# Kernel tuning notes

Measured on AMD Instinct MI355X. Metric: run time of the kernel, lower is better.

The kernel has to match this reference:

```python
import jax, jax.numpy as jnp
import numpy as np

C = 128         # sphere_channels
H = 512         # hidden_channels
EC = 128        # edge_channels
LMAX = 4
K = 4           # num_experts
N_EQ = 2        # ceil(K/2) equivariant experts
N_NE = 2
N_NODES = 8192
N_EDGES = 262144
DEG_SIZES = np.array([2 * l + 1 for l in range(LMAX + 1)])  # [1,3,5,7,9]
M = int(DEG_SIZES.sum())  # 25 coeffs


def setup_inputs() -> dict:
    key = jax.random.key(0)
    ks = jax.random.split(key, 20)
    s = 0.02
    return {
        "x_emb": jax.random.normal(ks[0], (N_NODES, M, C), jnp.float32),
        "t_ij": jax.random.normal(ks[1], (N_EDGES, EC), jnp.float32),
        "edge_index": jax.random.randint(ks[2], (2, N_EDGES), 0, N_NODES, jnp.int32),
        # equivariant experts (stacked on leading expert axis)
        "eq_w1": jax.random.normal(ks[3], (N_EQ, C, H), jnp.float32) * s,
        "eq_gate_w": jax.random.normal(ks[4], (N_EQ, EC, H * (LMAX + 1)), jnp.float32) * s,
        "eq_gate_b": jax.random.normal(ks[5], (N_EQ, H * (LMAX + 1)), jnp.float32) * s,
        "eq_w2": jax.random.normal(ks[6], (N_EQ, H, C), jnp.float32) * s,
        # non-equivariant experts
        "ne_w1": jax.random.normal(ks[7], (N_NE, C, H), jnp.float32) * s,
        "ne_b1": jax.random.normal(ks[8], (N_NE, H), jnp.float32) * s,
        "ne_gate_w": jax.random.normal(ks[9], (N_NE, EC, H), jnp.float32) * s,
        "ne_gate_b": jax.random.normal(ks[10], (N_NE, H), jnp.float32) * s,
        "ne_w2": jax.random.normal(ks[11], (N_NE, H, C), jnp.float32) * s,
        "ne_b2": jax.random.normal(ks[12], (N_NE, C), jnp.float32) * s,
        # router
        "r_w1": jax.random.normal(ks[13], (EC, EC), jnp.float32) * s,
        "r_b1": jax.random.normal(ks[14], (EC,), jnp.float32) * s,
        "r_w2": jax.random.normal(ks[15], (EC, K), jnp.float32) * s,
        "r_b2": jax.random.normal(ks[16], (K,), jnp.float32) * s,
    }


def reference(x_emb, t_ij, edge_index, eq_w1, eq_gate_w, eq_gate_b, eq_w2,
              ne_w1, ne_b1, ne_gate_w, ne_gate_b, ne_w2, ne_b2,
              r_w1, r_b1, r_w2, r_b2):
    N = x_emb.shape[0]
    silu = jax.nn.silu

    # c_i = scatter-mean of t_ij onto destination nodes
    dst = edge_index[1]
    sums = jax.ops.segment_sum(t_ij, dst, num_segments=N)
    cnt = jax.ops.segment_sum(jnp.ones((t_ij.shape[0],), t_ij.dtype), dst, num_segments=N)
    c = sums / jnp.maximum(cnt, 1.0)[:, None]  # [N, EC]

    # soft routing weights from context
    w = jax.nn.softmax(silu(c @ r_w1 + r_b1) @ r_w2 + r_b2, axis=-1)  # [N, K]

    repeats = jnp.asarray(DEG_SIZES)
    is_scalar = (jnp.arange(M) == 0)[:, None]  # l=0 coeff mask, [M,1]

    # --- equivariant experts (vectorized over expert axis e) ---
    h = jnp.einsum('nmc,ech->enmh', x_emb, eq_w1)                      # [e,N,M,H]
    g = silu(jnp.einsum('nc,ecg->eng', c, eq_gate_w) + eq_gate_b[:, None, :])
    g = g.reshape(N_EQ, N, LMAX + 1, H)
    g = jnp.repeat(g, repeats, axis=2, total_repeat_length=M)          # [e,N,M,H]
    h = jnp.where(is_scalar, silu(h), h) * g                           # SiLU only on l=0
    out_eq = jnp.einsum('enmh,ehc->enmc', h, eq_w2)

    # --- non-equivariant experts ---
    h2 = silu(jnp.einsum('nmc,ech->enmh', x_emb, ne_w1) + ne_b1[:, None, None, :])
    g2 = silu(jnp.einsum('nc,ech->enh', c, ne_gate_w) + ne_gate_b[:, None, :])
    h2 = h2 * g2[:, :, None, :]
    out_ne = jnp.einsum('enmh,ehc->enmc', h2, ne_w2) + ne_b2[:, None, None, :]

    # softmax-weighted mixture (equiv experts first, matching ModuleList order)
    out = (jnp.einsum('nk,knmc->nmc', w[:, :N_EQ], out_eq)
           + jnp.einsum('nk,knmc->nmc', w[:, N_EQ:], out_ne))
    return out
```

## Files before the change

kernel.cpp:

```cpp
#include <hip/hip_runtime.h>

#define NNODES 8192
#define NEDGES 262144
#define CCH    128
#define HCH    512
#define GCOLS  6144
#define ROWS   204800
#define XSPAD  136
#define HGPAD  72

typedef __bf16 bf16_t;
typedef __bf16 bf16x8 __attribute__((ext_vector_type(8)));
typedef __bf16 bf16x4 __attribute__((ext_vector_type(4)));
typedef float  f32x4  __attribute__((ext_vector_type(4)));

__device__ __forceinline__ float siluf(float x) {
  return x * __builtin_amdgcn_rcpf(1.f + __expf(-x));
}

#define GLOAD_LDS(g, l) __builtin_amdgcn_global_load_lds( \
    (const __attribute__((address_space(1))) void*)(g), \
    (__attribute__((address_space(3))) void*)(l), 16, 0, 0)

constexpr size_t OFF_CSUM  = 0;
constexpr size_t OFF_DEG   = 4194304;
constexpr size_t OFF_OFFS  = 4227072;
constexpr size_t OFF_CUR   = 4263936;
constexpr size_t OFF_EIDS  = 4296704;
constexpr size_t OFF_WRT   = 5345280;
constexpr size_t OFF_CBF   = 5476352;
constexpr size_t OFF_WPT   = 7573504;
constexpr size_t OFF_BPK   = 9146368;
constexpr size_t OFF_W1T   = 9170944;
constexpr size_t OFF_W2T   = 9695232;
constexpr size_t OFF_GATES = 10219520;

__global__ __launch_bounds__(256) void edge_count_kernel(
    const int* __restrict__ edge_index, int* __restrict__ deg)
{
  int e = blockIdx.x * 256 + threadIdx.x;
  int dst = __builtin_nontemporal_load(&edge_index[NEDGES + e]);
  atomicAdd(&deg[dst], 1);
}

__global__ __launch_bounds__(256) void scan_kernel(
    const int* __restrict__ deg, int* __restrict__ offs, int* __restrict__ cur)
{
  __shared__ int part[256];
  int t = threadIdx.x;
  int s = 0;
  #pragma unroll 4
  for (int i = 0; i < 32; ++i) s += deg[t * 32 + i];
  part[t] = s;
  __syncthreads();
  int incl = s;
  for (int off = 1; off < 256; off <<= 1) {
    int u = (t >= off) ? part[t - off] : 0;
    __syncthreads();
    incl += u;
    part[t] = incl;
    __syncthreads();
  }
  int run = incl - s;
  for (int i = 0; i < 32; ++i) {
    int d = deg[t * 32 + i];
    offs[t * 32 + i] = run;
    cur[t * 32 + i]  = run;
    run += d;
  }
  if (t == 255) offs[8192] = run;
}

__global__ __launch_bounds__(256) void edge_fill_kernel(
    const int* __restrict__ edge_index, int* __restrict__ cur, int* __restrict__ eids)
{
  int e = blockIdx.x * 256 + threadIdx.x;
  int dst = __builtin_nontemporal_load(&edge_index[NEDGES + e]);
  int pos = atomicAdd(&cur[dst], 1);
  eids[pos] = e;
}

__global__ __launch_bounds__(256) void gather_mean_kernel(
    const float* __restrict__ t_ij, const int* __restrict__ offs,
    const int* __restrict__ eids, float* __restrict__ csum, bf16_t* __restrict__ cbf)
{
  __shared__ float red[8][128];
  int n = blockIdx.x, tid = threadIdx.x;
  int sub = tid & 31, rp = tid >> 5;
  int o0 = offs[n], o1 = offs[n + 1];
  f32x4 acc = {0.f, 0.f, 0.f, 0.f};
  for (int j = o0 + rp; j < o1; j += 8) {
    int e = __builtin_nontemporal_load(&eids[j]);
    f32x4 v = __builtin_nontemporal_load((const f32x4*)&t_ij[(size_t)e * CCH + sub * 4]);
    #pragma unroll
    for (int q = 0; q < 4; ++q) acc[q] += v[q];
  }
  *(f32x4*)&red[rp][sub * 4] = acc;
  __syncthreads();
  if (rp == 0) {
    float inv = 1.f / fmaxf((float)(o1 - o0), 1.f);
    f32x4 s = {0.f, 0.f, 0.f, 0.f};
    #pragma unroll
    for (int k = 0; k < 8; ++k) {
      f32x4 r = *(const f32x4*)&red[k][sub * 4];
      #pragma unroll
      for (int q = 0; q < 4; ++q) s[q] += r[q];
    }
    f32x4 m;
    bf16x4 mb;
    #pragma unroll
    for (int q = 0; q < 4; ++q) { m[q] = s[q] * inv; mb[q] = (bf16_t)m[q]; }
    *(f32x4*)&csum[(size_t)n * CCH + sub * 4] = m;
    *(bf16x4*)&cbf[(size_t)n * CCH + sub * 4] = mb;
  }
}

__global__ __launch_bounds__(256) void pack_kernel(
    const float* __restrict__ eq_gate_w, const float* __restrict__ ne_gate_w,
    const float* __restrict__ eq_gate_b, const float* __restrict__ ne_gate_b,
    const float* __restrict__ eq_w1, const float* __restrict__ ne_w1,
    const float* __restrict__ eq_w2, const float* __restrict__ ne_w2,
    bf16_t* __restrict__ WpackT, float* __restrict__ bpack,
    bf16_t* __restrict__ w1T, bf16_t* __restrict__ w2c)
{
  __shared__ float tb[32][33];
  int b = blockIdx.x;
  int tid = threadIdx.x, tx = tid & 31, ty = tid >> 5;
  if (b == 1280) {
    #pragma unroll
    for (int it = 0; it < 24; ++it) {
      int j = it * 256 + tid;
      bpack[j] = (j < 5120) ? eq_gate_b[j] : ne_gate_b[j - 5120];
    }
    return;
  }
  const float* src; bf16_t* dst; int stride; bool w2mode = false;
  int c0, h0; size_t dbase;
  if (b < 640) {
    int e = b / 320, r = b % 320, ct = r / 80, ht = r % 80;
    src = eq_gate_w + (size_t)e * 327680; stride = 2560;
    c0 = ct * 32; h0 = ht * 32;
    dbase = ((size_t)e * 2560 + h0) * 128 + c0; dst = WpackT;
  } else if (b < 768) {
    int bb = b - 640, e = bb / 64, r = bb % 64, ct = r / 16, ht = r % 16;
    src = ne_gate_w + (size_t)e * 65536; stride = 512;
    c0 = ct * 32; h0 = ht * 32;
    dbase = ((size_t)(5120 + e * 512) + h0) * 128 + c0; dst = WpackT;
  } else if (b < 1024) {
    int bb = b - 768, e = bb / 64, r = bb % 64, ct = r / 16, ht = r % 16;
    src = (e < 2) ? eq_w1 + (size_t)e * 65536 : ne_w1 + (size_t)(e - 2) * 65536;
    stride = 512;
    c0 = ct * 32; h0 = ht * 32;
    dbase = ((size_t)(e * 512) + h0) * 128 + c0; dst = w1T;
  } else {
    int bb = b - 1024, e = bb / 64, r = bb % 64, ht = r / 4, ct = r % 4;
    src = (e < 2) ? eq_w2 + (size_t)e * 65536 : ne_w2 + (size_t)(e - 2) * 65536;
    stride = 128; w2mode = true;
    c0 = ct * 32; h0 = ht * 32;
    dbase = (size_t)e * 65536 + (size_t)(ht >> 1) * 8192 + (size_t)c0 * 64 + (size_t)(ht & 1) * 32;
    dst = w2c;
  }
  if (!w2mode) {
    #pragma unroll
    for (int p = 0; p < 4; ++p)
      tb[p * 8 + ty][tx] = src[(size_t)(c0 + p * 8 + ty) * stride + h0 + tx];
    __syncthreads();
    #pragma unroll
    for (int p = 0; p < 4; ++p)
      dst[dbase + (size_t)(p * 8 + ty) * 128 + tx] = (bf16_t)tb[tx][p * 8 + ty];
  } else {
    #pragma unroll
    for (int p = 0; p < 4; ++p)
      tb[p * 8 + ty][tx] = src[(size_t)(h0 + p * 8 + ty) * 128 + c0 + tx];
    __syncthreads();
    #pragma unroll
    for (int p = 0; p < 4; ++p)
      dst[dbase + (size_t)(p * 8 + ty) * 64 + tx] = (bf16_t)tb[tx][p * 8 + ty];
  }
}

__global__ __launch_bounds__(128) void router_kernel(
    const float* __restrict__ c,
    const float* __restrict__ r_w1, const float* __restrict__ r_b1,
    const float* __restrict__ r_w2, const float* __restrict__ r_b2,
    float* __restrict__ wroute)
{
  __shared__ float cl[128];
  __shared__ float h1[128];
  __shared__ float lg[4];
  int n = blockIdx.x, tid = threadIdx.x;
  cl[tid] = c[(size_t)n * 128 + tid];
  __syncthreads();
  float a = 0.f;
  #pragma unroll 8
  for (int k = 0; k < 128; ++k) a += cl[k] * r_w1[k * 128 + tid];
  a += r_b1[tid];
  h1[tid] = siluf(a);
  __syncthreads();
  if (tid < 4) {
    float s = 0.f;
    for (int j = 0; j < 128; ++j) s += h1[j] * r_w2[j * 4 + tid];
    lg[tid] = s + r_b2[tid];
  }
  __syncthreads();
  if (tid == 0) {
    float m = fmaxf(fmaxf(lg[0], lg[1]), fmaxf(lg[2], lg[3]));
    float e0 = __expf(lg[0] - m), e1 = __expf(lg[1] - m);
    float e2 = __expf(lg[2] - m), e3 = __expf(lg[3] - m);
    float s = 1.f / (e0 + e1 + e2 + e3);
    f32x4 w = {e0 * s, e1 * s, e2 * s, e3 * s};
    *(f32x4*)&wroute[n * 4] = w;
  }
}

__global__ __launch_bounds__(256, 2) void gate_gemm_kernel(
    const bf16_t* __restrict__ WpackT, const bf16_t* __restrict__ cbf,
    const float* __restrict__ bpack, const float* __restrict__ wroute,
    bf16_t* __restrict__ gates, int n0)
{
  __shared__ bf16_t gt[128 * XSPAD];
  int jt = blockIdx.x, nt = blockIdx.y;
  int tid = threadIdx.x;
  int wave = tid >> 6, lane = tid & 63;
  int wr = wave >> 1, wc = wave & 1;
  int l15 = lane & 15, quad = lane >> 4;
  int ej = (jt < 20) ? 0 : (jt < 40) ? 1 : (jt < 44) ? 2 : 3;

  f32x4 acc[4][4];
  #pragma unroll
  for (int i = 0; i < 4; ++i)
    #pragma unroll
    for (int j = 0; j < 4; ++j) acc[i][j] = {0.f, 0.f, 0.f, 0.f};

  const bf16_t* abase = WpackT + ((size_t)jt * 128 + wr * 64 + l15) * 128 + quad * 8;
  const bf16_t* bbase = cbf + ((size_t)(n0 + nt * 128) + wc * 64 + l15) * 128 + quad * 8;
  float wsc[4];
  #pragma unroll
  for (int tc = 0; tc < 4; ++tc)
    wsc[tc] = wroute[(size_t)(n0 + nt * 128 + wc * 64 + tc * 16 + l15) * 4 + ej];
  #pragma unroll
  for (int ks = 0; ks < 4; ++ks) {
    bf16x8 af[4], bfr[4];
    #pragma unroll
    for (int tr = 0; tr < 4; ++tr) af[tr] = *(const bf16x8*)(abase + (size_t)tr * 16 * 128 + ks * 32);
    #pragma unroll
    for (int tc = 0; tc < 4; ++tc) bfr[tc] = *(const bf16x8*)(bbase + (size_t)tc * 16 * 128 + ks * 32);
    #pragma unroll
    for (int tr = 0; tr < 4; ++tr)
      #pragma unroll
      for (int tc = 0; tc < 4; ++tc)
        acc[tr][tc] = __builtin_amdgcn_mfma_f32_16x16x32_bf16(af[tr], bfr[tc], acc[tr][tc], 0, 0, 0);
  }
  #pragma unroll
  for (int tr = 0; tr < 4; ++tr) {
    int j0 = wr * 64 + tr * 16 + quad * 4;
    int p0 = wr * 64 + quad * 16 + tr * 4;
    f32x4 bb = *(const f32x4*)&bpack[jt * 128 + j0];
    #pragma unroll
    for (int tc = 0; tc < 4; ++tc) {
      int nl = wc * 64 + tc * 16 + l15;
      f32x4 v = acc[tr][tc];
      bf16x4 gv;
      #pragma unroll
      for (int q = 0; q < 4; ++q) gv[q] = (bf16_t)(siluf(v[q] + bb[q]) * wsc[tc]);
      *(bf16x4*)&gt[nl * XSPAD + p0] = gv;
    }
  }
  __syncthreads();
  #pragma unroll
  for (int it = 0; it < 8; ++it) {
    int idx = it * 2048 + tid * 8;
    int lr = idx >> 7, col = idx & 127;
    *(bf16x8*)&gates[((size_t)nt * 128 + lr) * GCOLS + jt * 128 + col] =
        *(const bf16x8*)&gt[lr * XSPAD + col];
  }
}

__global__ __launch_bounds__(256, 2) void fused_experts_kernel(
    const float* __restrict__ x,
    const bf16_t* __restrict__ w1T,
    const bf16_t* __restrict__ w2c,
    const bf16_t* __restrict__ gates,
    const float* __restrict__ wroute,
    const float* __restrict__ ne_b1,
    const float* __restrict__ ne_b2,
    float* __restrict__ out,
    int n0)
{
  __shared__ __align__(16) bf16_t ws1[8192];
  __shared__ __align__(16) bf16_t ws2[8192];
  __shared__ __align__(16) bf16_t hg[4 * 32 * HGPAD];

  const int tid = threadIdx.x;
  const int wave = tid >> 6, lane = tid & 63;
  const int l15 = lane & 15, quad = lane >> 4;
  const int r0 = n0 * 25 + blockIdx.x * 128;
  const int rbase = wave * 32;
  bf16_t* hgw = hg + wave * 32 * HGPAD;

  int soff1[4], soff2[4];
  #pragma unroll
  for (int i = 0; i < 4; ++i) {
    int p = wave * 4096 + i * 1024 + lane * 16;
    int row1 = p >> 8;
    soff1[i] = (row1 * 256 + ((p & 255) ^ ((row1 & 7) << 4))) >> 1;
    int row2 = p >> 7;
    soff2[i] = (row2 * 128 + ((p & 127) ^ ((row2 & 7) << 4))) >> 1;
  }
  const int swz = (l15 & 7) << 4;
  int colswz[4];
  #pragma unroll
  for (int ks = 0; ks < 4; ++ks) colswz[ks] = (ks * 64 + quad * 16) ^ swz;

  int nloc[2], lidx[2];
  f32x4 rw[2];
  bf16x8 xf[2][4];
  #pragma unroll
  for (int tc = 0; tc < 2; ++tc) {
    int r = r0 + rbase + tc * 16 + l15;
    int n = r / 25;
    int m = r - n * 25;
    nloc[tc] = n - n0;
    lidx[tc] = (m == 0) ? 0 : (m < 4) ? 1 : (m < 9) ? 2 : (m < 16) ? 3 : 4;
    rw[tc] = *(const f32x4*)&wroute[n * 4];
    const float* xr = x + (size_t)r * CCH + quad * 8;
    #pragma unroll
    for (int ks = 0; ks < 4; ++ks) {
      f32x4 a = __builtin_nontemporal_load((const f32x4*)(xr + ks * 32));
      f32x4 b = __builtin_nontemporal_load((const f32x4*)(xr + ks * 32 + 4));
      bf16x8 v;
      #pragma unroll
      for (int q = 0; q < 4; ++q) { v[q] = (bf16_t)a[q]; v[4 + q] = (bf16_t)b[q]; }
      xf[tc][ks] = v;
    }
  }

  auto gaddr = [&](int tc, int tt) -> const bf16_t* {
    int ee = tt >> 3, hh = tt & 7;
    int base = (ee < 2) ? ee * 2560 + lidx[tc] * 512 : 5120 + (ee - 2) * 512;
    return gates + (nloc[tc] * GCOLS + base + hh * 64 + quad * 16);
  };

  f32x4 oacc[8][2];
  #pragma unroll
  for (int i = 0; i < 8; ++i)
    #pragma unroll
    for (int j = 0; j < 2; ++j) oacc[i][j] = {0.f, 0.f, 0.f, 0.f};

  bf16x8 gnxa[2], gnxb[2];
  #pragma unroll
  for (int tc = 0; tc < 2; ++tc) {
    const bf16_t* gp = gaddr(tc, 0);
    gnxa[tc] = *(const bf16x8*)gp;
    gnxb[tc] = *(const bf16x8*)(gp + 8);
  }
  #pragma unroll
  for (int i = 0; i < 4; ++i) {
    GLOAD_LDS(w1T + soff1[i], ws1 + wave * 2048 + i * 512);
    GLOAD_LDS(w2c + soff2[i], ws2 + wave * 2048 + i * 512);
  }
  __syncthreads();

  #pragma unroll 1
  for (int t = 0; t < 32; ++t) {
    const int e = t >> 3, hc = t & 7;
    const bool is_eq = (e < 2);

    bf16x8 ga[2], gb[2];
    #pragma unroll
    for (int tc = 0; tc < 2; ++tc) { ga[tc] = gnxa[tc]; gb[tc] = gnxb[tc]; }
    if (t < 31) {
      #pragma unroll
      for (int tc = 0; tc < 2; ++tc) {
        const bf16_t* gp = gaddr(tc, t + 1);
        gnxa[tc] = *(const bf16x8*)gp;
        gnxb[tc] = *(const bf16x8*)(gp + 8);
      }
    }

    f32x4 hacc[4][2];
    #pragma unroll
    for (int i = 0; i < 4; ++i)
      #pragma unroll
      for (int j = 0; j < 2; ++j) hacc[i][j] = {0.f, 0.f, 0.f, 0.f};
    #pragma unroll
    for (int ks = 0; ks < 4; ++ks) {
      bf16x8 af[4];
      #pragma unroll
      for (int tr = 0; tr < 4; ++tr)
        af[tr] = *(const bf16x8*)((const char*)ws1 + (l15 + tr * 16) * 256 + colswz[ks]);
      #pragma unroll
      for (int tr = 0; tr < 4; ++tr)
        #pragma unroll
        for (int tc = 0; tc < 2; ++tc)
          hacc[tr][tc] = __builtin_amdgcn_mfma_f32_16x16x32_bf16(af[tr], xf[tc][ks], hacc[tr][tc], 0, 0, 0);
    }
    #pragma unroll
    for (int tc = 0; tc < 2; ++tc) {
      #pragma unroll
      for (int tr = 0; tr < 4; ++tr) {
        int hl = tr * 16 + quad * 4;
        f32x4 v = hacc[tr][tc];
        if (is_eq) {
          if (lidx[tc] == 0) {
            #pragma unroll
            for (int q = 0; q < 4; ++q) v[q] = siluf(v[q]);
          }
        } else {
          f32x4 b1 = *(const f32x4*)&ne_b1[(e - 2) * 512 + hc * 64 + hl];
          #pragma unroll
          for (int q = 0; q < 4; ++q) v[q] = siluf(v[q] + b1[q]);
        }
        bf16x4 hv;
        #pragma unroll
        for (int q = 0; q < 4; ++q) {
          float gf = (float)((tr < 2 ? ga[tc] : gb[tc])[(tr & 1) * 4 + q]);
          hv[q] = (bf16_t)(v[q] * gf);
        }
        *(bf16x4*)&hgw[(tc * 16 + l15) * HGPAD + hl] = hv;
      }
    }
    __syncthreads();
    if (t < 31) {
      const bf16_t* g1 = w1T + ((size_t)(t + 1) << 13);
      #pragma unroll
      for (int i = 0; i < 4; ++i)
        GLOAD_LDS(g1 + soff1[i], ws1 + wave * 2048 + i * 512);
    }
    #pragma unroll
    for (int ks = 0; ks < 2; ++ks) {
      bf16x8 bfr[2];
      #pragma unroll
      for (int tc = 0; tc < 2; ++tc)
        bfr[tc] = *(const bf16x8*)&hgw[(tc * 16 + l15) * HGPAD + ks * 32 + quad * 8];
      #pragma unroll
      for (int tr = 0; tr < 8; ++tr) {
        bf16x8 af2 = *(const bf16x8*)((const char*)ws2 + (l15 + tr * 16) * 128 + colswz[ks]);
        #pragma unroll
        for (int tc = 0; tc < 2; ++tc)
          oacc[tr][tc] = __builtin_amdgcn_mfma_f32_16x16x32_bf16(af2, bfr[tc], oacc[tr][tc], 0, 0, 0);
      }
    }
    __syncthreads();
    if (t < 31) {
      const bf16_t* g2 = w2c + ((size_t)(t + 1) << 13);
      #pragma unroll
      for (int i = 0; i < 4; ++i)
        GLOAD_LDS(g2 + soff2[i], ws2 + wave * 2048 + i * 512);
    }
  }
  #pragma unroll
  for (int tc = 0; tc < 2; ++tc) {
    size_t rg = (size_t)(r0 + rbase + tc * 16 + l15);
    float wn0 = rw[tc][2], wn1 = rw[tc][3];
    #pragma unroll
    for (int tr = 0; tr < 8; ++tr) {
      int c0 = tr * 16 + quad * 4;
      f32x4 v = oacc[tr][tc];
      f32x4 b20 = *(const f32x4*)&ne_b2[c0];
      f32x4 b21 = *(const f32x4*)&ne_b2[128 + c0];
      f32x4 ov;
      #pragma unroll
      for (int q = 0; q < 4; ++q)
        ov[q] = v[q] + wn0 * b20[q] + wn1 * b21[q];
      __builtin_nontemporal_store(ov, (f32x4*)&out[rg * CCH + c0]);
    }
  }
}

extern "C" void kernel_launch(void* const* d_in, const int* in_sizes, int n_in,
                              void* d_out, int out_size, void* d_ws, size_t ws_size,
                              hipStream_t stream)
{
  const float* x_emb     = (const float*)d_in[0];
  const float* t_ij      = (const float*)d_in[1];
  const int*   edge_index= (const int*)d_in[2];
  const float* eq_w1     = (const float*)d_in[3];
  const float* eq_gate_w = (const float*)d_in[4];
  const float* eq_gate_b = (const float*)d_in[5];
  const float* eq_w2     = (const float*)d_in[6];
  const float* ne_w1     = (const float*)d_in[7];
  const float* ne_b1     = (const float*)d_in[8];
  const float* ne_gate_w = (const float*)d_in[9];
  const float* ne_gate_b = (const float*)d_in[10];
  const float* ne_w2     = (const float*)d_in[11];
  const float* ne_b2     = (const float*)d_in[12];
  const float* r_w1      = (const float*)d_in[13];
  const float* r_b1      = (const float*)d_in[14];
  const float* r_w2      = (const float*)d_in[15];
  const float* r_b2      = (const float*)d_in[16];
  float* out = (float*)d_out;

  char* ws = (char*)d_ws;
  float*  csum   = (float*)(ws + OFF_CSUM);
  int*    deg    = (int*)(ws + OFF_DEG);
  int*    offs   = (int*)(ws + OFF_OFFS);
  int*    cur    = (int*)(ws + OFF_CUR);
  int*    eids   = (int*)(ws + OFF_EIDS);
  float*  wroute = (float*)(ws + OFF_WRT);
  bf16_t* cbf    = (bf16_t*)(ws + OFF_CBF);
  bf16_t* WpackT = (bf16_t*)(ws + OFF_WPT);
  float*  bpack  = (float*)(ws + OFF_BPK);
  bf16_t* w1T    = (bf16_t*)(ws + OFF_W1T);
  bf16_t* w2c    = (bf16_t*)(ws + OFF_W2T);
  bf16_t* gates  = (bf16_t*)(ws + OFF_GATES);

  size_t avail = (ws_size > OFF_GATES) ? ws_size - OFF_GATES : 0;
  int chunk = 128;
  for (int c = NNODES; c >= 128; c >>= 1) {
    if ((size_t)c * GCOLS * sizeof(bf16_t) <= avail) { chunk = c; break; }
  }

  hipMemsetAsync(ws + OFF_DEG, 0, 32768, stream);

  edge_count_kernel<<<NEDGES / 256, 256, 0, stream>>>(edge_index, deg);
  scan_kernel<<<1, 256, 0, stream>>>(deg, offs, cur);
  edge_fill_kernel<<<NEDGES / 256, 256, 0, stream>>>(edge_index, cur, eids);
  gather_mean_kernel<<<NNODES, 256, 0, stream>>>(t_ij, offs, eids, csum, cbf);

  pack_kernel<<<1281, 256, 0, stream>>>(eq_gate_w, ne_gate_w, eq_gate_b, ne_gate_b,
                                        eq_w1, ne_w1, eq_w2, ne_w2,
                                        WpackT, bpack, w1T, w2c);
  router_kernel<<<NNODES, 128, 0, stream>>>(csum, r_w1, r_b1, r_w2, r_b2, wroute);

  for (int n0 = 0; n0 < NNODES; n0 += chunk) {
    gate_gemm_kernel<<<dim3(GCOLS / 128, chunk / 128), 256, 0, stream>>>(
        WpackT, cbf, bpack, wroute, gates, n0);
    fused_experts_kernel<<<chunk * 25 / 128, 256, 0, stream>>>(
        x_emb, w1T, w2c, gates, wroute, ne_b1, ne_b2, out, n0);
  }
}
```

Before: 783.9 us.

## Fuse router into gather-mean kernel and interleave gating epilogue with second GEMM

Folds the router MLP and softmax into the scatter-mean kernel, so the per-node mean stays in shared memory and is no longer written to and re-read from global memory. This also removes one 8192-block launch. Separately, the SiLU and gating epilogue of the expert kernel is split into two halves, each placed just before the matching k-step of the second MFMA GEMM, so it can overlap the weight prefetch. The risks are higher register pressure in the expert kernel and half the threads idling during the fused router phase.

```diff
diff --git a/kernel.cpp b/kernel.cpp
--- a/kernel.cpp
+++ b/kernel.cpp
@@ -80,11 +80,17 @@
   eids[pos] = e;
 }
 
-__global__ __launch_bounds__(256) void gather_mean_kernel(
+__global__ __launch_bounds__(256) void gather_mean_router_kernel(
     const float* __restrict__ t_ij, const int* __restrict__ offs,
-    const int* __restrict__ eids, float* __restrict__ csum, bf16_t* __restrict__ cbf)
+    const int* __restrict__ eids,
+    const float* __restrict__ r_w1, const float* __restrict__ r_b1,
+    const float* __restrict__ r_w2, const float* __restrict__ r_b2,
+    bf16_t* __restrict__ cbf, float* __restrict__ wroute)
 {
   __shared__ float red[8][128];
+  __shared__ float mm[128];
+  __shared__ float h1s[128];
+  __shared__ float lg[4];
   int n = blockIdx.x, tid = threadIdx.x;
   int sub = tid & 31, rp = tid >> 5;
   int o0 = offs[n], o1 = offs[n + 1];
@@ -110,8 +116,30 @@
     bf16x4 mb;
     #pragma unroll
     for (int q = 0; q < 4; ++q) { m[q] = s[q] * inv; mb[q] = (bf16_t)m[q]; }
-    *(f32x4*)&csum[(size_t)n * CCH + sub * 4] = m;
+    *(f32x4*)&mm[sub * 4] = m;
     *(bf16x4*)&cbf[(size_t)n * CCH + sub * 4] = mb;
+  }
+  __syncthreads();
+  if (tid < 128) {
+    float a = r_b1[tid];
+    #pragma unroll 8
+    for (int k = 0; k < 128; ++k) a += mm[k] * r_w1[k * 128 + tid];
+    h1s[tid] = siluf(a);
+  }
+  __syncthreads();
+  if (tid < 4) {
+    float s2 = r_b2[tid];
+    for (int j = 0; j < 128; ++j) s2 += h1s[j] * r_w2[j * 4 + tid];
+    lg[tid] = s2;
+  }
+  __syncthreads();
+  if (tid == 0) {
+    float m = fmaxf(fmaxf(lg[0], lg[1]), fmaxf(lg[2], lg[3]));
+    float e0 = __expf(lg[0] - m), e1 = __expf(lg[1] - m);
+    float e2 = __expf(lg[2] - m), e3 = __expf(lg[3] - m);
+    float s = 1.f / (e0 + e1 + e2 + e3);
+    f32x4 w = {e0 * s, e1 * s, e2 * s, e3 * s};
+    *(f32x4*)&wroute[n * 4] = w;
   }
 }
 
@@ -179,40 +207,6 @@
   }
 }
 
-__global__ __launch_bounds__(128) void router_kernel(
-    const float* __restrict__ c,
-    const float* __restrict__ r_w1, const float* __restrict__ r_b1,
-    const float* __restrict__ r_w2, const float* __restrict__ r_b2,
-    float* __restrict__ wroute)
-{
-  __shared__ float cl[128];
-  __shared__ float h1[128];
-  __shared__ float lg[4];
-  int n = blockIdx.x, tid = threadIdx.x;
-  cl[tid] = c[(size_t)n * 128 + tid];
-  __syncthreads();
-  float a = 0.f;
-  #pragma unroll 8
-  for (int k = 0; k < 128; ++k) a += cl[k] * r_w1[k * 128 + tid];
-  a += r_b1[tid];
-  h1[tid] = siluf(a);
-  __syncthreads();
-  if (tid < 4) {
-    float s = 0.f;
-    for (int j = 0; j < 128; ++j) s += h1[j] * r_w2[j * 4 + tid];
-    lg[tid] = s + r_b2[tid];
-  }
-  __syncthreads();
-  if (tid == 0) {
-    float m = fmaxf(fmaxf(lg[0], lg[1]), fmaxf(lg[2], lg[3]));
-    float e0 = __expf(lg[0] - m), e1 = __expf(lg[1] - m);
-    float e2 = __expf(lg[2] - m), e3 = __expf(lg[3] - m);
-    float s = 1.f / (e0 + e1 + e2 + e3);
-    f32x4 w = {e0 * s, e1 * s, e2 * s, e3 * s};
-    *(f32x4*)&wroute[n * 4] = w;
-  }
-}
-
 __global__ __launch_bounds__(256, 2) void gate_gemm_kernel(
     const bf16_t* __restrict__ WpackT, const bf16_t* __restrict__ cbf,
     const float* __restrict__ bpack, const float* __restrict__ wroute,
@@ -395,31 +389,6 @@
         for (int tc = 0; tc < 2; ++tc)
           hacc[tr][tc] = __builtin_amdgcn_mfma_f32_16x16x32_bf16(af[tr], xf[tc][ks], hacc[tr][tc], 0, 0, 0);
     }
-    #pragma unroll
-    for (int tc = 0; tc < 2; ++tc) {
-      #pragma unroll
-      for (int tr = 0; tr < 4; ++tr) {
-        int hl = tr * 16 + quad * 4;
-        f32x4 v = hacc[tr][tc];
-        if (is_eq) {
-          if (lidx[tc] == 0) {
-            #pragma unroll
-            for (int q = 0; q < 4; ++q) v[q] = siluf(v[q]);
-          }
-        } else {
-          f32x4 b1 = *(const f32x4*)&ne_b1[(e - 2) * 512 + hc * 64 + hl];
-          #pragma unroll
-          for (int q = 0; q < 4; ++q) v[q] = siluf(v[q] + b1[q]);
-        }
-        bf16x4 hv;
-        #pragma unroll
-        for (int q = 0; q < 4; ++q) {
-          float gf = (float)((tr < 2 ? ga[tc] : gb[tc])[(tr & 1) * 4 + q]);
-          hv[q] = (bf16_t)(v[q] * gf);
-        }
-        *(bf16x4*)&hgw[(tc * 16 + l15) * HGPAD + hl] = hv;
-      }
-    }
     __syncthreads();
     if (t < 31) {
       const bf16_t* g1 = w1T + ((size_t)(t + 1) << 13);
@@ -428,14 +397,40 @@
         GLOAD_LDS(g1 + soff1[i], ws1 + wave * 2048 + i * 512);
     }
     #pragma unroll
-    for (int ks = 0; ks < 2; ++ks) {
+    for (int half = 0; half < 2; ++half) {
+      #pragma unroll
+      for (int tc = 0; tc < 2; ++tc) {
+        #pragma unroll
+        for (int trh = 0; trh < 2; ++trh) {
+          int tr = half * 2 + trh;
+          int hl = tr * 16 + quad * 4;
+          f32x4 v = hacc[tr][tc];
+          if (is_eq) {
+            if (lidx[tc] == 0) {
+              #pragma unroll
+              for (int q = 0; q < 4; ++q) v[q] = siluf(v[q]);
+            }
+          } else {
+            f32x4 b1 = *(const f32x4*)&ne_b1[(e - 2) * 512 + hc * 64 + hl];
+            #pragma unroll
+            for (int q = 0; q < 4; ++q) v[q] = siluf(v[q] + b1[q]);
+          }
+          bf16x4 hv;
+          #pragma unroll
+          for (int q = 0; q < 4; ++q) {
+            float gf = (float)((half == 0 ? ga[tc] : gb[tc])[trh * 4 + q]);
+            hv[q] = (bf16_t)(v[q] * gf);
+          }
+          *(bf16x4*)&hgw[(tc * 16 + l15) * HGPAD + hl] = hv;
+        }
+      }
       bf16x8 bfr[2];
       #pragma unroll
       for (int tc = 0; tc < 2; ++tc)
-        bfr[tc] = *(const bf16x8*)&hgw[(tc * 16 + l15) * HGPAD + ks * 32 + quad * 8];
+        bfr[tc] = *(const bf16x8*)&hgw[(tc * 16 + l15) * HGPAD + half * 32 + quad * 8];
       #pragma unroll
       for (int tr = 0; tr < 8; ++tr) {
-        bf16x8 af2 = *(const bf16x8*)((const char*)ws2 + (l15 + tr * 16) * 128 + colswz[ks]);
+        bf16x8 af2 = *(const bf16x8*)((const char*)ws2 + (l15 + tr * 16) * 128 + colswz[half]);
         #pragma unroll
         for (int tc = 0; tc < 2; ++tc)
           oacc[tr][tc] = __builtin_amdgcn_mfma_f32_16x16x32_bf16(af2, bfr[tc], oacc[tr][tc], 0, 0, 0);
@@ -492,7 +487,6 @@
   float* out = (float*)d_out;
 
   char* ws = (char*)d_ws;
-  float*  csum   = (float*)(ws + OFF_CSUM);
   int*    deg    = (int*)(ws + OFF_DEG);
   int*    offs   = (int*)(ws + OFF_OFFS);
   int*    cur    = (int*)(ws + OFF_CUR);
@@ -516,12 +510,12 @@
   edge_count_kernel<<<NEDGES / 256, 256, 0, stream>>>(edge_index, deg);
   scan_kernel<<<1, 256, 0, stream>>>(deg, offs, cur);
   edge_fill_kernel<<<NEDGES / 256, 256, 0, stream>>>(edge_index, cur, eids);
-  gather_mean_kernel<<<NNODES, 256, 0, stream>>>(t_ij, offs, eids, csum, cbf);
+  gather_mean_router_kernel<<<NNODES, 256, 0, stream>>>(
+      t_ij, offs, eids, r_w1, r_b1, r_w2, r_b2, cbf, wroute);
 
   pack_kernel<<<1281, 256, 0, stream>>>(eq_gate_w, ne_gate_w, eq_gate_b, ne_gate_b,
                                         eq_w1, ne_w1, eq_w2, ne_w2,
                                         WpackT, bpack, w1T, w2c);
-  router_kernel<<<NNODES, 128, 0, stream>>>(csum, r_w1, r_b1, r_w2, r_b2, wroute);
 
   for (int n0 = 0; n0 < NNODES; n0 += chunk) {
     gate_gemm_kernel<<<dim3(GCOLS / 128, chunk / 128), 256, 0, stream>>>(
```

After: 766.1 us. 2.3% less time.
